# Optimization experiments

Hardware: AMD Instinct MI355X
Metric: run time of the kernel (lower is better)

Reference implementation:

```python
import jax, jax.numpy as jnp
import numpy as np

EPS = 1e-9


def setup_inputs() -> dict:
    key = jax.random.key(0)
    k1, k2, k3 = jax.random.split(key, 3)
    B, N, E, F_IN, F_OUT = 8, 2048, 1024, 256, 256
    x = jax.random.normal(k1, (B, N, F_IN), dtype=jnp.float32)
    H = jax.random.uniform(k2, (B, N, E), dtype=jnp.float32)  # soft incidence matrix
    weight = jax.random.normal(k3, (F_IN, F_OUT), dtype=jnp.float32) * (1.0 / np.sqrt(F_OUT))
    return {"x": x, "H": H, "weight": weight}


def reference(x, H, weight):
    # x: [B, N, Fin], H: [B, N, E], weight: [Fin, Fout]
    # Torch builds diag_embed(Dv_inv)/diag_embed(De_inv) and uses dense bmm;
    # mathematically identical to elementwise row-scaling, done here directly.
    Dv = jnp.sum(H, axis=2)                       # [B, N]  (= bmm(H, ones))
    De = jnp.sum(H, axis=1)                       # [B, E]
    Dv_inv = 1.0 / (Dv + EPS)
    De_inv = 1.0 / (De + EPS)
    xw = jnp.matmul(x, weight)                    # [B, N, Fout]
    HTX = jnp.einsum('bne,bnf->bef', H, xw)       # H^T @ X
    HDeHTX = jnp.einsum('bne,bef->bnf', H, De_inv[:, :, None] * HTX)
    out = Dv_inv[:, :, None] * HDeHTX             # [B, N, Fout]
    # dropout in eval mode (identity); relu kept
    return jax.nn.relu(out)
```

## Files before the change

kernel.cpp:

```cpp
#include <hip/hip_runtime.h>
#include <stdint.h>


typedef __bf16 bf16x8 __attribute__((ext_vector_type(8)));
typedef float f32x4 __attribute__((ext_vector_type(4)));

__device__ __forceinline__ uint16_t f2b(float f) {
  __bf16 h = (__bf16)f;
  return __builtin_bit_cast(uint16_t, h);
}

__device__ __forceinline__ f32x4 mfma16(bf16x8 a, bf16x8 b, f32x4 c) {
  return __builtin_amdgcn_mfma_f32_16x16x32_bf16(a, b, c, 0, 0, 0);
}

__device__ __forceinline__ void gload16(const void* src, void* dst) {
  __builtin_amdgcn_global_load_lds(
      (const __attribute__((address_space(1))) void*)src,
      (__attribute__((address_space(3))) void*)dst, 16, 0, 0);
}

#define PIPE_WAIT4() do { \
    asm volatile("s_waitcnt vmcnt(4)" ::: "memory"); \
    __builtin_amdgcn_s_barrier(); \
    __builtin_amdgcn_sched_barrier(0); \
  } while (0)
#define PIPE_WAIT0() do { \
    asm volatile("s_waitcnt vmcnt(0)" ::: "memory"); \
    __builtin_amdgcn_s_barrier(); \
    __builtin_amdgcn_sched_barrier(0); \
  } while (0)

__global__ __launch_bounds__(256) void k_prep_w(const float* __restrict__ W,
    uint16_t* __restrict__ Wt) {
  __shared__ __align__(16) uint16_t T[64 * 68];
  const int k0 = blockIdx.x * 64, f0 = blockIdx.y * 64;
  const int t = threadIdx.x;
  const int r0 = (t >> 4) * 4, cc = (t & 15) * 4;
  float vv[4][4];
  #pragma unroll
  for (int i = 0; i < 4; ++i) {
    float4 q = *(const float4*)(W + (size_t)(k0 + r0 + i) * 256 + f0 + cc);
    vv[i][0] = q.x; vv[i][1] = q.y; vv[i][2] = q.z; vv[i][3] = q.w;
  }
  #pragma unroll
  for (int j = 0; j < 4; ++j) {
    union { uint16_t s[4]; uint2 u; } p;
    #pragma unroll
    for (int i = 0; i < 4; ++i) p.s[i] = f2b(vv[i][j]);
    *(uint2*)&T[(cc + j) * 68 + r0] = p.u;
  }
  __syncthreads();
  const int er = t >> 2, c2 = (t & 3) * 16;
  union { uint16_t s[16]; uint4 q[2]; } o;
  #pragma unroll
  for (int m = 0; m < 4; ++m)
    *(uint2*)&o.s[m * 4] = *(const uint2*)&T[er * 68 + c2 + m * 4];
  uint16_t* dst = Wt + (size_t)(f0 + er) * 256 + k0 + c2;
  *(uint4*)dst = o.q[0];
  *(uint4*)(dst + 8) = o.q[1];
}

__global__ __launch_bounds__(256) void k_phase1(const float* __restrict__ H,
    const float* __restrict__ X, const uint16_t* __restrict__ Wt,
    uint16_t* __restrict__ Hb, float* __restrict__ DvInv,
    float* __restrict__ DePart, uint16_t* __restrict__ XWt) {
  __shared__ __align__(16) unsigned char smem[17408];
  const int lin = blockIdx.x;
  const int t = threadIdx.x, lane = t & 63, wave = t >> 6;

  if (lin < 1024) {
    float* dvp = (float*)smem;
    const int nb = lin & 127, b = lin >> 7;
    const int n0 = nb * 16;
    const float* Hrow = H + ((size_t)b * 2048 + n0) * 1024 + t * 4;
    uint16_t* HbRow = Hb + ((size_t)b * 2048 + n0) * 1024 + t * 4;
    float de0 = 0.f, de1 = 0.f, de2 = 0.f, de3 = 0.f;
    #pragma unroll
    for (int g = 0; g < 4; ++g) {
      float4 q[4];
      #pragma unroll
      for (int i = 0; i < 4; ++i)
        q[i] = *(const float4*)(Hrow + (size_t)(g * 4 + i) * 1024);
      #pragma unroll
      for (int i = 0; i < 4; ++i) {
        const int r = g * 4 + i;
        de0 += q[i].x; de1 += q[i].y; de2 += q[i].z; de3 += q[i].w;
        float rs = (q[i].x + q[i].y) + (q[i].z + q[i].w);
        rs += __shfl_xor(rs, 1);  rs += __shfl_xor(rs, 2);
        rs += __shfl_xor(rs, 4);  rs += __shfl_xor(rs, 8);
        rs += __shfl_xor(rs, 16); rs += __shfl_xor(rs, 32);
        if (lane == 0) dvp[r * 4 + wave] = rs;
        union { uint16_t s[4]; uint2 u; } p;
        p.s[0] = f2b(q[i].x); p.s[1] = f2b(q[i].y);
        p.s[2] = f2b(q[i].z); p.s[3] = f2b(q[i].w);
        *(uint2*)(HbRow + (size_t)r * 1024) = p.u;
      }
    }
    *(float4*)(DePart + ((size_t)b * 128 + nb) * 1024 + t * 4) =
        make_float4(de0, de1, de2, de3);
    __syncthreads();
    if (t < 16) {
      float s = (dvp[t * 4 + 0] + dvp[t * 4 + 1]) + (dvp[t * 4 + 2] + dvp[t * 4 + 3]);
      DvInv[b * 2048 + n0 + t] = 1.f / (s + 1e-9f);
    }
  } else {
    uint16_t* As = (uint16_t*)smem;
    uint16_t* Bs = (uint16_t*)(smem + 8192);
    const int l1 = lin - 1024;
    const int n0 = (l1 & 31) * 64, f0 = ((l1 >> 5) & 3) * 64, b = l1 >> 7;
    const int l15 = lane & 15, lq = lane >> 4;
    const int rlane = lane >> 3;
    const int srcswz = ((lane & 7) ^ rlane) << 3;
    const uint16_t* Ag = Wt + (size_t)f0 * 256;
    const int br = t >> 2, kc = (t & 3) * 16;
    const float* Xg = X + ((size_t)b * 2048 + n0 + br) * 256 + kc;
    f32x4 acc[2][2] = {};
    for (int kt = 0; kt < 4; ++kt) {
      if (kt) __syncthreads();
      const int k0 = kt * 64;
      #pragma unroll
      for (int i = 0; i < 2; ++i) {
        const int r = wave * 16 + i * 8;
        gload16(Ag + (size_t)(r + rlane) * 256 + k0 + srcswz, As + r * 64);
      }
      {
        float4 RX[4];
        const float* s = Xg + k0;
        #pragma unroll
        for (int q = 0; q < 4; ++q) RX[q] = *(const float4*)(s + q * 4);
        uint16_t* d = Bs + br * 72 + kc;
        const float* f = (const float*)RX;
        #pragma unroll
        for (int q = 0; q < 2; ++q) {
          union { uint16_t s[8]; uint4 u; } p;
          #pragma unroll
          for (int j = 0; j < 8; ++j) p.s[j] = f2b(f[q * 8 + j]);
          *(uint4*)(d + q * 8) = p.u;
        }
      }
      __syncthreads();
      #pragma unroll
      for (int h = 0; h < 2; ++h) {
        bf16x8 af[2], bf[2];
        #pragma unroll
        for (int i = 0; i < 2; ++i) {
          const int r = (wave >> 1) * 32 + i * 16 + l15;
          af[i] = *(const bf16x8*)(As + r * 64 + ((((h << 2) | lq) ^ (r & 7)) << 3));
        }
        #pragma unroll
        for (int j = 0; j < 2; ++j) {
          const int r = (wave & 1) * 32 + j * 16 + l15;
          bf[j] = *(const bf16x8*)(Bs + r * 72 + h * 32 + lq * 8);
        }
        #pragma unroll
        for (int i = 0; i < 2; ++i)
          #pragma unroll
          for (int j = 0; j < 2; ++j)
            acc[i][j] = mfma16(af[i], bf[j], acc[i][j]);
      }
    }
    #pragma unroll
    for (int i = 0; i < 2; ++i) {
      const int fr = f0 + (wave >> 1) * 32 + i * 16 + lq * 4;
      #pragma unroll
      for (int j = 0; j < 2; ++j) {
        const int col = n0 + (wave & 1) * 32 + j * 16 + l15;
        #pragma unroll
        for (int reg = 0; reg < 4; ++reg)
          XWt[((size_t)b * 256 + fr + reg) * 2048 + col] = f2b(acc[i][j][reg]);
      }
    }
  }
}

__global__ __launch_bounds__(256) void k_gemm2(const uint16_t* __restrict__ Hb,
    const uint16_t* __restrict__ XWt, const float* __restrict__ DePart,
    uint16_t* __restrict__ Yt) {
  __shared__ __align__(16) uint16_t As[3][64 * 64];
  __shared__ __align__(16) uint16_t Bsm[2][64 * 72];
  __shared__ float sde4[64][4];
  __shared__ float sde[64];
  const int e0 = blockIdx.x * 64, f0 = blockIdx.y * 64, b = blockIdx.z;
  const int t = threadIdx.x, lane = t & 63, wave = t >> 6;
  const int l15 = lane & 15, lq = lane >> 4;
  const int rlane = lane >> 3;
  const int srcswz = ((lane & 7) ^ rlane) << 3;
  const uint16_t* Ag = XWt + ((size_t)b * 256 + f0) * 2048;
  const int br0 = (t >> 4) * 4;
  const int bcc = (t & 15) * 4;
  const uint16_t* Bgb = Hb + (size_t)b * 2048 * 1024 + e0 + bcc;
  auto stageA = [&](uint16_t* Ad, int kt) {
    const int k0 = kt * 64;
    #pragma unroll
    for (int i = 0; i < 2; ++i) {
      const int r = wave * 16 + i * 8;
      gload16(Ag + (size_t)(r + rlane) * 2048 + k0 + srcswz, Ad + r * 64);
    }
  };
  auto loadB = [&](uint2* R, int kt) {
    const uint16_t* s = Bgb + (size_t)(kt * 64 + br0) * 1024;
    #pragma unroll
    for (int i = 0; i < 4; ++i) R[i] = *(const uint2*)(s + (size_t)i * 1024);
  };
  auto writeB = [&](uint16_t* Bd, const uint2* R) {
    #pragma unroll
    for (int j = 0; j < 4; ++j) {
      union { uint16_t s[4]; uint2 u; } p;
      #pragma unroll
      for (int i = 0; i < 4; ++i) p.s[i] = ((const uint16_t*)&R[i])[j];
      *(uint2*)&Bd[(bcc + j) * 72 + br0] = p.u;
    }
  };
  f32x4 acc[2][2] = {};
  auto compute = [&](const uint16_t* Ad, const uint16_t* Bd) {
    #pragma unroll
    for (int h = 0; h < 2; ++h) {
      bf16x8 af[2], bf[2];
      #pragma unroll
      for (int i = 0; i < 2; ++i) {
        const int r = (wave >> 1) * 32 + i * 16 + l15;
        af[i] = *(const bf16x8*)(Ad + r * 64 + ((((h << 2) | lq) ^ (r & 7)) << 3));
      }
      #pragma unroll
      for (int j = 0; j < 2; ++j) {
        const int r = (wave & 1) * 32 + j * 16 + l15;
        bf[j] = *(const bf16x8*)(Bd + r * 72 + h * 32 + lq * 8);
      }
      #pragma unroll
      for (int i = 0; i < 2; ++i)
        #pragma unroll
        for (int j = 0; j < 2; ++j)
          acc[i][j] = mfma16(af[i], bf[j], acc[i][j]);
    }
  };
  {
    const float* p = DePart + (size_t)b * 128 * 1024 + (t >> 6) * 32 * 1024
                   + e0 + (t & 63);
    float s = 0.f;
    #pragma unroll
    for (int q = 0; q < 32; ++q) s += p[(size_t)q * 1024];
    sde4[t & 63][t >> 6] = s;
  }
  uint2 RB0[4], RB1[4];
  loadB(RB0, 0);
  stageA(As[0], 0);
  stageA(As[1], 1);
  asm volatile("s_waitcnt vmcnt(4)" ::: "memory");
  writeB(Bsm[0], RB0);
  loadB(RB1, 1);
  asm volatile("s_waitcnt vmcnt(6) lgkmcnt(0)" ::: "memory");
  __builtin_amdgcn_s_barrier();
  __builtin_amdgcn_sched_barrier(0);
  if (t < 64)
    sde[t] = 1.f / (((sde4[t][0] + sde4[t][1]) + (sde4[t][2] + sde4[t][3])) + 1e-9f);
  const int NT = 32;
  uint16_t *cA = As[0], *nA = As[1], *fA = As[2];
  #define G2_STEP(KT, RBH, RBF, BSC, BSN)                                    \
    do {                                                                     \
      stageA(fA, (KT) + 2);                                                  \
      loadB(RBF, (KT) + 2);                                                  \
      compute(cA, BSC);                                                      \
      asm volatile("s_waitcnt vmcnt(6)" ::: "memory");                       \
      writeB(BSN, RBH);                                                      \
      asm volatile("s_waitcnt lgkmcnt(0)" ::: "memory");                     \
      __builtin_amdgcn_s_barrier();                                          \
      __builtin_amdgcn_sched_barrier(0);                                     \
      uint16_t* tp = cA; cA = nA; nA = fA; fA = tp;                          \
    } while (0)
  for (int kt = 0; kt < NT - 2; kt += 2) {
    G2_STEP(kt,     RB1, RB0, Bsm[0], Bsm[1]);
    G2_STEP(kt + 1, RB0, RB1, Bsm[1], Bsm[0]);
  }
  #undef G2_STEP
  compute(cA, Bsm[0]);
  asm volatile("s_waitcnt vmcnt(0)" ::: "memory");
  writeB(Bsm[1], RB1);
  asm volatile("s_waitcnt lgkmcnt(0)" ::: "memory");
  __builtin_amdgcn_s_barrier();
  __builtin_amdgcn_sched_barrier(0);
  compute(nA, Bsm[1]);
  #pragma unroll
  for (int i = 0; i < 2; ++i) {
    const int fr = f0 + (wave >> 1) * 32 + i * 16 + lq * 4;
    #pragma unroll
    for (int j = 0; j < 2; ++j) {
      const int el = (wave & 1) * 32 + j * 16 + l15;
      const float sc = sde[el];
      uint16_t* dst = Yt + ((size_t)b * 256 + fr) * 1024 + e0 + el;
      #pragma unroll
      for (int reg = 0; reg < 4; ++reg)
        dst[(size_t)reg * 1024] = f2b(acc[i][j][reg] * sc);
    }
  }
}

__global__ __launch_bounds__(256) void k_gemm3(const uint16_t* __restrict__ Hb,
    const uint16_t* __restrict__ Yt, const float* __restrict__ DvInv,
    float* __restrict__ out) {
  __shared__ __align__(16) uint16_t As[3][64 * 64];
  __shared__ __align__(16) uint16_t Bs[3][64 * 64];
  __shared__ float sdv[64];
  const int n0 = blockIdx.x * 64, f0 = blockIdx.y * 64, b = blockIdx.z;
  const int t = threadIdx.x, lane = t & 63, wave = t >> 6;
  const int l15 = lane & 15, lq = lane >> 4;
  const int rlane = lane >> 3;
  const int srcswz = ((lane & 7) ^ rlane) << 3;
  const uint16_t* Ag = Hb + ((size_t)b * 2048 + n0) * 1024;
  const uint16_t* Bg = Yt + ((size_t)b * 256 + f0) * 1024;
  auto stage = [&](uint16_t* Ad, uint16_t* Bd, int kt) {
    const int k0 = kt * 64;
    #pragma unroll
    for (int i = 0; i < 2; ++i) {
      const int r = wave * 16 + i * 8;
      gload16(Ag + (size_t)(r + rlane) * 1024 + k0 + srcswz, Ad + r * 64);
      gload16(Bg + (size_t)(r + rlane) * 1024 + k0 + srcswz, Bd + r * 64);
    }
  };
  f32x4 acc[2][2] = {};
  auto compute = [&](const uint16_t* Ad, const uint16_t* Bd) {
    #pragma unroll
    for (int h = 0; h < 2; ++h) {
      bf16x8 af[2], bf[2];
      #pragma unroll
      for (int i = 0; i < 2; ++i) {
        const int r = (wave >> 1) * 32 + i * 16 + l15;
        af[i] = *(const bf16x8*)(Ad + r * 64 + ((((h << 2) | lq) ^ (r & 7)) << 3));
      }
      #pragma unroll
      for (int j = 0; j < 2; ++j) {
        const int r = (wave & 1) * 32 + j * 16 + l15;
        bf[j] = *(const bf16x8*)(Bd + r * 64 + ((((h << 2) | lq) ^ (r & 7)) << 3));
      }
      #pragma unroll
      for (int i = 0; i < 2; ++i)
        #pragma unroll
        for (int j = 0; j < 2; ++j)
          acc[i][j] = mfma16(af[i], bf[j], acc[i][j]);
    }
  };
  if (t < 64) sdv[t] = DvInv[b * 2048 + n0 + t];
  stage(As[0], Bs[0], 0);
  stage(As[1], Bs[1], 1);
  __syncthreads();
  const int NT = 16;
  uint16_t *cA = As[0], *nA = As[1], *fA = As[2];
  uint16_t *cB = Bs[0], *nB = Bs[1], *fB = Bs[2];
  for (int kt = 0; kt < NT - 2; ++kt) {
    stage(fA, fB, kt + 2);
    compute(cA, cB);
    PIPE_WAIT4();
    uint16_t* t1 = cA; cA = nA; nA = fA; fA = t1;
    uint16_t* t2 = cB; cB = nB; nB = fB; fB = t2;
  }
  compute(cA, cB);
  PIPE_WAIT0();
  compute(nA, nB);
  #pragma unroll
  for (int i = 0; i < 2; ++i) {
    const int nl = (wave >> 1) * 32 + i * 16 + lq * 4;
    #pragma unroll
    for (int reg = 0; reg < 4; ++reg) {
      const int row = n0 + nl + reg;
      const float sc = sdv[nl + reg];
      #pragma unroll
      for (int j = 0; j < 2; ++j) {
        const int col = f0 + (wave & 1) * 32 + j * 16 + l15;
        const float v = acc[i][j][reg] * sc;
        out[((size_t)b * 2048 + row) * 256 + col] = v > 0.f ? v : 0.f;
      }
    }
  }
}

extern "C" void kernel_launch(void* const* d_in, const int* in_sizes, int n_in,
                              void* d_out, int out_size, void* d_ws, size_t ws_size,
                              hipStream_t stream) {
  (void)in_sizes; (void)n_in; (void)out_size;
  const float* x = (const float*)d_in[0];
  const float* H = (const float*)d_in[1];
  const float* W = (const float*)d_in[2];
  float* out = (float*)d_out;

  if (ws_size < 50528256) return;
  char* ws = (char*)d_ws;
  uint16_t* Hb     = (uint16_t*)(ws);
  uint16_t* XWt    = (uint16_t*)(ws + 33554432);
  uint16_t* Yt     = (uint16_t*)(ws + 41943040);
  float*    DvInv  = (float*)(ws + 46137344);
  float*    DePart = (float*)(ws + 46202880);
  uint16_t* Wt     = (uint16_t*)(ws + 50397184);

  k_prep_w<<<dim3(4, 4),     256, 0, stream>>>(W, Wt);
  k_phase1<<<dim3(2048),     256, 0, stream>>>(H, x, Wt, Hb, DvInv, DePart, XWt);
  k_gemm2 <<<dim3(16, 4, 8), 256, 0, stream>>>(Hb, XWt, DePart, Yt);
  k_gemm3 <<<dim3(32, 4, 8), 256, 0, stream>>>(Hb, Yt, DvInv, out);
}
```

Baseline: 82.14 us.

## Compute degree sums with ones-vector MFMAs inside the GEMMs instead of a reduction pass

Removes the row and column sum reductions, the DePart partial buffer and the DvInv buffer from phase1. Instead, the edge degree (De) and vertex degree (Dv) are computed on the matrix cores by multiplying the bf16 H tiles already in shared memory against a ones vector inside gemm2 and gemm3. This drops shuffle reductions, extra global writes and reads, and a strided DePart reduction, at the cost of extra MFMAs per step. Degrees are now summed from bf16-rounded H rather than the fp32 inputs, which slightly changes numerics.

```diff
diff --git a/kernel.cpp b/kernel.cpp
--- a/kernel.cpp
+++ b/kernel.cpp
@@ -12,6 +12,12 @@
 
 __device__ __forceinline__ f32x4 mfma16(bf16x8 a, bf16x8 b, f32x4 c) {
   return __builtin_amdgcn_mfma_f32_16x16x32_bf16(a, b, c, 0, 0, 0);
+}
+
+__device__ __forceinline__ bf16x8 ones8() {
+  __bf16 one = (__bf16)1.0f;
+  bf16x8 v = {one, one, one, one, one, one, one, one};
+  return v;
 }
 
 __device__ __forceinline__ void gload16(const void* src, void* dst) {
@@ -63,46 +69,29 @@
 
 __global__ __launch_bounds__(256) void k_phase1(const float* __restrict__ H,
     const float* __restrict__ X, const uint16_t* __restrict__ Wt,
-    uint16_t* __restrict__ Hb, float* __restrict__ DvInv,
-    float* __restrict__ DePart, uint16_t* __restrict__ XWt) {
+    uint16_t* __restrict__ Hb, uint16_t* __restrict__ XWt) {
   __shared__ __align__(16) unsigned char smem[17408];
   const int lin = blockIdx.x;
   const int t = threadIdx.x, lane = t & 63, wave = t >> 6;
 
   if (lin < 1024) {
-    float* dvp = (float*)smem;
     const int nb = lin & 127, b = lin >> 7;
     const int n0 = nb * 16;
     const float* Hrow = H + ((size_t)b * 2048 + n0) * 1024 + t * 4;
     uint16_t* HbRow = Hb + ((size_t)b * 2048 + n0) * 1024 + t * 4;
-    float de0 = 0.f, de1 = 0.f, de2 = 0.f, de3 = 0.f;
-    #pragma unroll
-    for (int g = 0; g < 4; ++g) {
-      float4 q[4];
-      #pragma unroll
-      for (int i = 0; i < 4; ++i)
-        q[i] = *(const float4*)(Hrow + (size_t)(g * 4 + i) * 1024);
-      #pragma unroll
-      for (int i = 0; i < 4; ++i) {
-        const int r = g * 4 + i;
-        de0 += q[i].x; de1 += q[i].y; de2 += q[i].z; de3 += q[i].w;
-        float rs = (q[i].x + q[i].y) + (q[i].z + q[i].w);
-        rs += __shfl_xor(rs, 1);  rs += __shfl_xor(rs, 2);
-        rs += __shfl_xor(rs, 4);  rs += __shfl_xor(rs, 8);
-        rs += __shfl_xor(rs, 16); rs += __shfl_xor(rs, 32);
-        if (lane == 0) dvp[r * 4 + wave] = rs;
+    #pragma unroll
+    for (int g = 0; g < 2; ++g) {
+      float4 q[8];
+      #pragma unroll
+      for (int i = 0; i < 8; ++i)
+        q[i] = *(const float4*)(Hrow + (size_t)(g * 8 + i) * 1024);
+      #pragma unroll
+      for (int i = 0; i < 8; ++i) {
         union { uint16_t s[4]; uint2 u; } p;
         p.s[0] = f2b(q[i].x); p.s[1] = f2b(q[i].y);
         p.s[2] = f2b(q[i].z); p.s[3] = f2b(q[i].w);
-        *(uint2*)(HbRow + (size_t)r * 1024) = p.u;
-      }
-    }
-    *(float4*)(DePart + ((size_t)b * 128 + nb) * 1024 + t * 4) =
-        make_float4(de0, de1, de2, de3);
-    __syncthreads();
-    if (t < 16) {
-      float s = (dvp[t * 4 + 0] + dvp[t * 4 + 1]) + (dvp[t * 4 + 2] + dvp[t * 4 + 3]);
-      DvInv[b * 2048 + n0 + t] = 1.f / (s + 1e-9f);
+        *(uint2*)(HbRow + (size_t)(g * 8 + i) * 1024) = p.u;
+      }
     }
   } else {
     uint16_t* As = (uint16_t*)smem;
@@ -175,17 +164,15 @@
 }
 
 __global__ __launch_bounds__(256) void k_gemm2(const uint16_t* __restrict__ Hb,
-    const uint16_t* __restrict__ XWt, const float* __restrict__ DePart,
-    uint16_t* __restrict__ Yt) {
+    const uint16_t* __restrict__ XWt, uint16_t* __restrict__ Yt) {
   __shared__ __align__(16) uint16_t As[3][64 * 64];
   __shared__ __align__(16) uint16_t Bsm[2][64 * 72];
-  __shared__ float sde4[64][4];
-  __shared__ float sde[64];
   const int e0 = blockIdx.x * 64, f0 = blockIdx.y * 64, b = blockIdx.z;
   const int t = threadIdx.x, lane = t & 63, wave = t >> 6;
   const int l15 = lane & 15, lq = lane >> 4;
   const int rlane = lane >> 3;
   const int srcswz = ((lane & 7) ^ rlane) << 3;
+  const bf16x8 ONES = ones8();
   const uint16_t* Ag = XWt + ((size_t)b * 256 + f0) * 2048;
   const int br0 = (t >> 4) * 4;
   const int bcc = (t & 15) * 4;
@@ -213,6 +200,7 @@
     }
   };
   f32x4 acc[2][2] = {};
+  f32x4 acc_de[2] = {};
   auto compute = [&](const uint16_t* Ad, const uint16_t* Bd) {
     #pragma unroll
     for (int h = 0; h < 2; ++h) {
@@ -232,16 +220,11 @@
         #pragma unroll
         for (int j = 0; j < 2; ++j)
           acc[i][j] = mfma16(af[i], bf[j], acc[i][j]);
-    }
-  };
-  {
-    const float* p = DePart + (size_t)b * 128 * 1024 + (t >> 6) * 32 * 1024
-                   + e0 + (t & 63);
-    float s = 0.f;
-    #pragma unroll
-    for (int q = 0; q < 32; ++q) s += p[(size_t)q * 1024];
-    sde4[t & 63][t >> 6] = s;
-  }
+      #pragma unroll
+      for (int j = 0; j < 2; ++j)
+        acc_de[j] = mfma16(ONES, bf[j], acc_de[j]);
+    }
+  };
   uint2 RB0[4], RB1[4];
   loadB(RB0, 0);
   stageA(As[0], 0);
@@ -252,8 +235,6 @@
   asm volatile("s_waitcnt vmcnt(6) lgkmcnt(0)" ::: "memory");
   __builtin_amdgcn_s_barrier();
   __builtin_amdgcn_sched_barrier(0);
-  if (t < 64)
-    sde[t] = 1.f / (((sde4[t][0] + sde4[t][1]) + (sde4[t][2] + sde4[t][3])) + 1e-9f);
   const int NT = 32;
   uint16_t *cA = As[0], *nA = As[1], *fA = As[2];
   #define G2_STEP(KT, RBH, RBF, BSC, BSN)                                    \
@@ -286,7 +267,7 @@
     #pragma unroll
     for (int j = 0; j < 2; ++j) {
       const int el = (wave & 1) * 32 + j * 16 + l15;
-      const float sc = sde[el];
+      const float sc = 1.f / (acc_de[j][0] + 1e-9f);
       uint16_t* dst = Yt + ((size_t)b * 256 + fr) * 1024 + e0 + el;
       #pragma unroll
       for (int reg = 0; reg < 4; ++reg)
@@ -296,16 +277,15 @@
 }
 
 __global__ __launch_bounds__(256) void k_gemm3(const uint16_t* __restrict__ Hb,
-    const uint16_t* __restrict__ Yt, const float* __restrict__ DvInv,
-    float* __restrict__ out) {
+    const uint16_t* __restrict__ Yt, float* __restrict__ out) {
   __shared__ __align__(16) uint16_t As[3][64 * 64];
   __shared__ __align__(16) uint16_t Bs[3][64 * 64];
-  __shared__ float sdv[64];
   const int n0 = blockIdx.x * 64, f0 = blockIdx.y * 64, b = blockIdx.z;
   const int t = threadIdx.x, lane = t & 63, wave = t >> 6;
   const int l15 = lane & 15, lq = lane >> 4;
   const int rlane = lane >> 3;
   const int srcswz = ((lane & 7) ^ rlane) << 3;
+  const bf16x8 ONES = ones8();
   const uint16_t* Ag = Hb + ((size_t)b * 2048 + n0) * 1024;
   const uint16_t* Bg = Yt + ((size_t)b * 256 + f0) * 1024;
   auto stage = [&](uint16_t* Ad, uint16_t* Bd, int kt) {
@@ -318,6 +298,7 @@
     }
   };
   f32x4 acc[2][2] = {};
+  f32x4 acc_dv[2] = {};
   auto compute = [&](const uint16_t* Ad, const uint16_t* Bd) {
     #pragma unroll
     for (int h = 0; h < 2; ++h) {
@@ -337,9 +318,11 @@
         #pragma unroll
         for (int j = 0; j < 2; ++j)
           acc[i][j] = mfma16(af[i], bf[j], acc[i][j]);
-    }
-  };
-  if (t < 64) sdv[t] = DvInv[b * 2048 + n0 + t];
+      #pragma unroll
+      for (int i = 0; i < 2; ++i)
+        acc_dv[i] = mfma16(af[i], ONES, acc_dv[i]);
+    }
+  };
   stage(As[0], Bs[0], 0);
   stage(As[1], Bs[1], 1);
   __syncthreads();
@@ -362,7 +345,7 @@
     #pragma unroll
     for (int reg = 0; reg < 4; ++reg) {
       const int row = n0 + nl + reg;
-      const float sc = sdv[nl + reg];
+      const float sc = 1.f / (acc_dv[i][reg] + 1e-9f);
       #pragma unroll
       for (int j = 0; j < 2; ++j) {
         const int col = f0 + (wave & 1) * 32 + j * 16 + l15;
@@ -382,17 +365,15 @@
   const float* W = (const float*)d_in[2];
   float* out = (float*)d_out;
 
-  if (ws_size < 50528256) return;
+  if (ws_size < 46268416) return;
   char* ws = (char*)d_ws;
-  uint16_t* Hb     = (uint16_t*)(ws);
-  uint16_t* XWt    = (uint16_t*)(ws + 33554432);
-  uint16_t* Yt     = (uint16_t*)(ws + 41943040);
-  float*    DvInv  = (float*)(ws + 46137344);
-  float*    DePart = (float*)(ws + 46202880);
-  uint16_t* Wt     = (uint16_t*)(ws + 50397184);
+  uint16_t* Hb  = (uint16_t*)(ws);
+  uint16_t* XWt = (uint16_t*)(ws + 33554432);
+  uint16_t* Yt  = (uint16_t*)(ws + 41943040);
+  uint16_t* Wt  = (uint16_t*)(ws + 46137344);
 
   k_prep_w<<<dim3(4, 4),     256, 0, stream>>>(W, Wt);
-  k_phase1<<<dim3(2048),     256, 0, stream>>>(H, x, Wt, Hb, DvInv, DePart, XWt);
-  k_gemm2 <<<dim3(16, 4, 8), 256, 0, stream>>>(Hb, XWt, DePart, Yt);
-  k_gemm3 <<<dim3(32, 4, 8), 256, 0, stream>>>(Hb, Yt, DvInv, out);
-}
+  k_phase1<<<dim3(2048),     256, 0, stream>>>(H, x, Wt, Hb, XWt);
+  k_gemm2 <<<dim3(16, 4, 8), 256, 0, stream>>>(Hb, XWt, Yt);
+  k_gemm3 <<<dim3(32, 4, 8), 256, 0, stream>>>(Hb, Yt, out);
+}
```

Measured after the change: 82.39 us. About the same (+0.3%).
